# Optimization experiments

Hardware: AMD Instinct MI355X
Metric: run time of the kernel (lower is better)

Reference implementation:

```python
import jax, jax.numpy as jnp
import numpy as np

B, K_SLOTS, P = 4096, 8, 768
SLOT = P // 3          # 256, slot feature dim
HID = 256              # pres/up hidden width
NC, NP = 512, 512
LN_EPS = 1e-5


def _layernorm(x, g, b):
    m = jnp.mean(x, axis=-1, keepdims=True)
    v = jnp.var(x, axis=-1, keepdims=True)
    return (x - m) * jax.lax.rsqrt(v + LN_EPS) * g + b


def _mlp2(x, W1, b1, g, bt, W2, b2):
    # Linear -> LayerNorm -> ReLU -> Linear (torchvision ops.MLP with hidden=[256, out])
    h = jax.nn.relu(_layernorm(x @ W1 + b1, g, bt))
    return h @ W2 + b2


def setup_inputs() -> dict:
    key = jax.random.key(0)
    ks = jax.random.split(key, 24)
    rn = lambda k, shp, s=1.0: jax.random.normal(k, shp, dtype=jnp.float32) * s
    d = {
        "inst_embed": rn(ks[0], (B, P)),
        "slots": rn(ks[1], (B, K_SLOTS, SLOT)),
        # fc / fp: single Linear(p, p)
        "Wfc": rn(ks[2], (P, P), 1.0 / np.sqrt(P)),
        "bfc": jnp.zeros((P,), jnp.float32),
        "Wfp": rn(ks[3], (P, P), 1.0 / np.sqrt(P)),
        "bfp": jnp.zeros((P,), jnp.float32),
        # memory codebooks (plain randn per the original)
        "Kc": rn(ks[4], (NC, P)),
        "Vc": rn(ks[5], (NC, P)),
        "Kp": rn(ks[6], (NP, P)),
        "Vp": rn(ks[7], (NP, P)),
        # pres MLP: Linear(4p/3,256)+LN+ReLU, Linear(256,p/3)
        "pres_W1": rn(ks[8], (SLOT + P, HID), 1.0 / np.sqrt(SLOT + P)),
        "pres_b1": jnp.zeros((HID,), jnp.float32),
        "pres_g": jnp.ones((HID,), jnp.float32),
        "pres_bt": jnp.zeros((HID,), jnp.float32),
        "pres_W2": rn(ks[9], (HID, SLOT), 1.0 / np.sqrt(HID)),
        "pres_b2": jnp.zeros((SLOT,), jnp.float32),
        # up MLP: same shapes
        "up_W1": rn(ks[10], (SLOT + P, HID), 1.0 / np.sqrt(SLOT + P)),
        "up_b1": jnp.zeros((HID,), jnp.float32),
        "up_g": jnp.ones((HID,), jnp.float32),
        "up_bt": jnp.zeros((HID,), jnp.float32),
        "up_W2": rn(ks[11], (HID, SLOT), 1.0 / np.sqrt(HID)),
        "up_b2": jnp.zeros((SLOT,), jnp.float32),
    }
    return d


def reference(inst_embed, slots, Wfc, bfc, Wfp, bfp, Kc, Vc, Kp, Vp,
              pres_W1, pres_b1, pres_g, pres_bt, pres_W2, pres_b2,
              up_W1, up_b1, up_g, up_bt, up_W2, up_b2):
    scale = jnp.float32(np.sqrt(P))
    # selection: soft attention over the two codebooks
    Qc = inst_embed @ Wfc + bfc                     # [B, P]
    Qp = inst_embed @ Wfp + bfp                     # [B, P]
    c = jax.nn.softmax(jnp.einsum('bi,ci->bc', Qc, Kc) / scale, axis=-1) @ Vc  # [B, P]
    p = jax.nn.softmax(jnp.einsum('bi,pi->bp', Qp, Kp) / scale, axis=-1) @ Vp  # [B, P]
    # update: vectorized over the K slot loop of the original
    cb = jnp.broadcast_to(c[:, None, :], (B, K_SLOTS, P))
    pb = jnp.broadcast_to(p[:, None, :], (B, K_SLOTS, P))
    hc = jnp.concatenate([slots, cb], axis=-1)      # [B, K, SLOT+P]
    hp = jnp.concatenate([slots, pb], axis=-1)      # [B, K, SLOT+P]
    gate_pres = _mlp2(hc, pres_W1, pres_b1, pres_g, pres_bt, pres_W2, pres_b2)
    gate_up = _mlp2(hp, up_W1, up_b1, up_g, up_bt, up_W2, up_b2)
    return slots + gate_pres * gate_up              # [B, K, SLOT]
```

## Files before the change

kernel.cpp:

```cpp
#include <hip/hip_runtime.h>
#include <stdint.h>

#define BB    4096
#define KS    8
#define PP    768
#define SLOT  256
#define HID   256
#define NC    512
#define BKROWS (BB*KS)
typedef unsigned short u16;
typedef short bf16x8 __attribute__((ext_vector_type(8)));
typedef float f32x4  __attribute__((ext_vector_type(4)));

__device__ __forceinline__ u16 f2bf(float x) {
  union { float f; uint32_t u; } v; v.f = x;
  return (u16)((v.u + 0x7FFFu + ((v.u >> 16) & 1u)) >> 16);
}

__device__ __forceinline__ u16 f2h(float x) {
  union { _Float16 h; u16 u; } cv; cv.h = (_Float16)x; return cv.u;
}
__device__ __forceinline__ float h2f(u16 x) {
  union { u16 u; _Float16 h; } cv; cv.u = x; return (float)cv.h;
}

__device__ __forceinline__ void gload_lds16(u16* ldst, const u16* gsrc) {
  __builtin_amdgcn_global_load_lds(
      (const __attribute__((address_space(1))) void*)gsrc,
      (__attribute__((address_space(3))) void*)ldst, 16, 0, 0);
}

template<int EPI>
__device__ __forceinline__ void gemm_core6464(
    const u16* __restrict__ A, int lda,
    const u16* __restrict__ B, int ldb,
    const float* __restrict__ bias,
    void* __restrict__ out, int ldo, int K,
    int blockRow, int blockCol, u16* lsA, u16* lsB)
{
  const int tid  = threadIdx.x;
  const int w    = tid >> 6;
  const int lane = tid & 63;
  const int wm   = w >> 1, wn = w & 1;
  const int rl   = lane >> 4, cl = lane & 15;

  f32x4 acc[2][2];
  const f32x4 zero = {0.f, 0.f, 0.f, 0.f};
#pragma unroll
  for (int i = 0; i < 2; ++i)
#pragma unroll
    for (int j = 0; j < 2; ++j) acc[i][j] = zero;

  const u16* Ablk = A + (size_t)blockRow * lda;
  const u16* Bblk = B + (size_t)blockCol * ldb;

  for (int k0 = 0; k0 < K; k0 += 64) {
#pragma unroll
    for (int i = 0; i < 2; ++i) {
      int seg   = i * 4 + w;
      int off16 = seg * 64 + lane;
      int row   = off16 >> 3;
      int chunk = (off16 & 7) ^ (row & 7);
      gload_lds16(lsA + seg * 512, Ablk + (size_t)row * lda + k0 + chunk * 8);
    }
#pragma unroll
    for (int i = 0; i < 2; ++i) {
      int seg   = i * 4 + w;
      int off16 = seg * 64 + lane;
      int row   = off16 >> 3;
      int chunk = (off16 & 7) ^ (row & 7);
      gload_lds16(lsB + seg * 512, Bblk + (size_t)row * ldb + k0 + chunk * 8);
    }
    __syncthreads();

#pragma unroll
    for (int ks = 0; ks < 2; ++ks) {
      bf16x8 aF[2], bF[2];
#pragma unroll
      for (int f = 0; f < 2; ++f) {
        int r  = wm * 32 + f * 16 + cl;
        int ca = ((ks * 4 + rl) ^ (r & 7)) * 8;
        aF[f] = *(const bf16x8*)(lsA + r * 64 + ca);
        int rn = wn * 32 + f * 16 + cl;
        int cb = ((ks * 4 + rl) ^ (rn & 7)) * 8;
        bF[f] = *(const bf16x8*)(lsB + rn * 64 + cb);
      }
#pragma unroll
      for (int fm = 0; fm < 2; ++fm)
#pragma unroll
        for (int fn = 0; fn < 2; ++fn)
          acc[fm][fn] = __builtin_amdgcn_mfma_f32_16x16x32_bf16(
              aF[fm], bF[fn], acc[fm][fn], 0, 0, 0);
    }
    __syncthreads();
  }

#pragma unroll
  for (int fm = 0; fm < 2; ++fm) {
#pragma unroll
    for (int fn = 0; fn < 2; ++fn) {
      f32x4 v = acc[fm][fn];
#pragma unroll
      for (int r = 0; r < 4; ++r) {
        int grow = blockRow + wm * 32 + fm * 16 + rl * 4 + r;
        int gcol = blockCol + wn * 32 + fn * 16 + cl;
        float x = v[r];
        if constexpr (EPI == 2) {
          ((u16*)out)[(size_t)grow * ldo + gcol] = f2bf(x);
        } else if constexpr (EPI == 3) {
          x += bias[gcol];
          ((float*)out)[(size_t)grow * ldo + gcol] = x;
        } else if constexpr (EPI == 5) {
          x += bias[gcol];
          ((u16*)out)[(size_t)grow * ldo + gcol] = f2h(x);
        }
      }
    }
  }
}

__device__ __forceinline__ void cvt_seg(const float* __restrict__ in,
                                        u16* __restrict__ outp, int b, int n4) {
  int i = b * 256 + threadIdx.x;
  if (i < n4) {
    float4 v = ((const float4*)in)[i];
    ushort4 o;
    o.x = f2bf(v.x); o.y = f2bf(v.y); o.z = f2bf(v.z); o.w = f2bf(v.w);
    ((ushort4*)outp)[i] = o;
  }
}

__device__ __forceinline__ void pack_seg(const float* __restrict__ s0,
                                         const float* __restrict__ s1,
                                         u16* __restrict__ dst, int b) {
  int br = b >> 4, ng = b & 15;
  const float* src = br ? s1 : s0;
  int w = threadIdx.x >> 6, lane = threadIdx.x & 63;
  int rl = lane >> 4, cl = lane & 15;
#pragma unroll
  for (int s = 0; s < 2; ++s) {
    int step = w * 2 + s;
    union { u16 u[8]; uint4 q; } o;
#pragma unroll
    for (int j = 0; j < 8; ++j)
      o.u[j] = f2bf(src[(size_t)(step * 32 + rl * 8 + j) * 256 + ng * 16 + cl]);
    *(uint4*)(dst + (size_t)(((br * 16 + ng) * 8 + step) * 64 + lane) * 8) = o.q;
  }
}

__global__ __launch_bounds__(256) void prep_all(
    const float* __restrict__ Kc, const float* __restrict__ Kp,
    const float* __restrict__ Wfc, const float* __restrict__ Wfp,
    const float* __restrict__ Vc, const float* __restrict__ Vp,
    const float* __restrict__ pW1, const float* __restrict__ uW1,
    const float* __restrict__ pW2, const float* __restrict__ uW2,
    const float* __restrict__ bfc, const float* __restrict__ bfp,
    u16* Kcb, u16* Kpb, u16* Wfcb, u16* Wfpb, u16* Vcb, u16* Vpb,
    u16* W1Tp, u16* W1Tu, u16* W1pk, u16* W2pk, float* sb)
{
  __shared__ float tile[32][33];
  int b = blockIdx.x;
  if (b < 384)       { cvt_seg(Kc,   Kcb,   b,         98304); return; }
  else if (b < 768)  { cvt_seg(Kp,   Kpb,   b - 384,   98304); return; }
  else if (b < 1344) { cvt_seg(Wfc,  Wfcb,  b - 768,  147456); return; }
  else if (b < 1920) { cvt_seg(Wfp,  Wfpb,  b - 1344, 147456); return; }
  else if (b < 2304) { cvt_seg(Vc,   Vcb,   b - 1920,  98304); return; }
  else if (b < 2688) { cvt_seg(Vp,   Vpb,   b - 2304,  98304); return; }
  else if (b < 3200) {
    int bb = b - 2688;
    const float* in = (bb < 256) ? pW1 : uW1;
    u16* outp = (bb < 256) ? W1Tp : W1Tu;
    bb &= 255;
    int tc = (bb & 7) * 32, tr = (bb >> 3) * 32;
    int lx = threadIdx.x & 31, ly = threadIdx.x >> 5;
#pragma unroll
    for (int i = 0; i < 32; i += 8)
      tile[ly + i][lx] = in[(size_t)(tr + ly + i) * 256 + tc + lx];
    __syncthreads();
#pragma unroll
    for (int i = 0; i < 32; i += 8)
      outp[(size_t)(tc + ly + i) * 1024 + tr + lx] = f2bf(tile[lx][ly + i]);
    return;
  }
  else if (b < 3232) { pack_seg(pW1, uW1, W1pk, b - 3200); return; }
  else if (b < 3264) { pack_seg(pW2, uW2, W2pk, b - 3232); return; }
  else {
    int w = threadIdx.x >> 6, lane = threadIdx.x & 63;
    int row = (b - 3264) * 4 + w;
    int br = row >> 9, n = row & 511;
    const float* Kr = (br ? Kp : Kc) + (size_t)n * PP;
    const float* bf = br ? bfp : bfc;
    float s = 0.f;
#pragma unroll
    for (int j = 0; j < 12; ++j) s += Kr[lane + j * 64] * bf[lane + j * 64];
#pragma unroll
    for (int o = 32; o; o >>= 1) s += __shfl_xor(s, o);
    if (!lane) sb[row] = s;
  }
}

__global__ __launch_bounds__(256) void gemm_mixed(
    const u16* Kcb, const u16* Kpb, const u16* Wfcb, const u16* Wfpb,
    u16* KWc, u16* KWp,
    const u16* W1Tp, const u16* W1Tu, const u16* Vcb, const u16* Vpb,
    u16* VW1p, u16* VW1u)
{
  __shared__ u16 lsA[64 * 64];
  __shared__ u16 lsB[64 * 64];
  int b = blockIdx.x;
  if (b < 192) {
    int z = b / 96, r = b % 96;
    gemm_core6464<2>(z ? Kpb : Kcb, PP, z ? Wfpb : Wfcb, PP, nullptr,
                     z ? KWp : KWc, PP, PP, (r & 7) * 64, (r >> 3) * 64, lsA, lsB);
  } else {
    int c = b - 192, z = c / 32, r = c % 32;
    gemm_core6464<2>((z ? W1Tu : W1Tp) + 256, 1024, z ? Vpb : Vcb, PP, nullptr,
                     z ? VW1u : VW1p, NC, PP, (r & 3) * 64, (r >> 2) * 64, lsA, lsB);
  }
}

__global__ __launch_bounds__(256) void gemm_scores(
    const float* __restrict__ inst, const u16* __restrict__ KW,
    const float* __restrict__ sb, u16* __restrict__ scH)
{
  __shared__ u16 lsA[64 * 64];
  __shared__ u16 lsB[64 * 64];
  const int tid  = threadIdx.x;
  const int w    = tid >> 6;
  const int lane = tid & 63;
  const int wm   = w >> 1, wn = w & 1;
  const int rl   = lane >> 4, cl = lane & 15;
  const int blockRow = blockIdx.x * 64;
  const int blockCol = blockIdx.y * 64;

  const int arow = tid >> 2;
  const int kseg = (tid & 3) * 16;

  f32x4 acc[2][2];
  const f32x4 zero = {0.f, 0.f, 0.f, 0.f};
#pragma unroll
  for (int i = 0; i < 2; ++i)
#pragma unroll
    for (int j = 0; j < 2; ++j) acc[i][j] = zero;

  const float* Asrc = inst + (size_t)(blockRow + arow) * PP + kseg;
  const u16*   Bblk = KW + (size_t)blockCol * PP;

  for (int k0 = 0; k0 < PP; k0 += 64) {
    union { u16 u[8]; uint4 q; } c0, c1;
#pragma unroll
    for (int j = 0; j < 2; ++j) {
      float4 v0 = *(const float4*)(Asrc + k0 + j * 8);
      float4 v1 = *(const float4*)(Asrc + k0 + j * 8 + 4);
      u16* dd = j ? c1.u : c0.u;
      dd[0] = f2bf(v0.x); dd[1] = f2bf(v0.y); dd[2] = f2bf(v0.z); dd[3] = f2bf(v0.w);
      dd[4] = f2bf(v1.x); dd[5] = f2bf(v1.y); dd[6] = f2bf(v1.z); dd[7] = f2bf(v1.w);
    }
    int cc = kseg >> 3;
    *(uint4*)(lsA + arow * 64 + (((cc     ) ^ (arow & 7)) << 3)) = c0.q;
    *(uint4*)(lsA + arow * 64 + (((cc + 1) ^ (arow & 7)) << 3)) = c1.q;
#pragma unroll
    for (int i = 0; i < 2; ++i) {
      int seg   = i * 4 + w;
      int off16 = seg * 64 + lane;
      int row   = off16 >> 3;
      int chunk = (off16 & 7) ^ (row & 7);
      gload_lds16(lsB + seg * 512, Bblk + (size_t)row * PP + k0 + chunk * 8);
    }
    __syncthreads();

#pragma unroll
    for (int ks = 0; ks < 2; ++ks) {
      bf16x8 aF[2], bF[2];
#pragma unroll
      for (int f = 0; f < 2; ++f) {
        int r  = wm * 32 + f * 16 + cl;
        int ca = ((ks * 4 + rl) ^ (r & 7)) * 8;
        aF[f] = *(const bf16x8*)(lsA + r * 64 + ca);
        int rn = wn * 32 + f * 16 + cl;
        int cb = ((ks * 4 + rl) ^ (rn & 7)) * 8;
        bF[f] = *(const bf16x8*)(lsB + rn * 64 + cb);
      }
#pragma unroll
      for (int fm = 0; fm < 2; ++fm)
#pragma unroll
        for (int fn = 0; fn < 2; ++fn)
          acc[fm][fn] = __builtin_amdgcn_mfma_f32_16x16x32_bf16(
              aF[fm], bF[fn], acc[fm][fn], 0, 0, 0);
    }
    __syncthreads();
  }

#pragma unroll
  for (int fm = 0; fm < 2; ++fm)
#pragma unroll
    for (int fn = 0; fn < 2; ++fn) {
      f32x4 v = acc[fm][fn];
#pragma unroll
      for (int r = 0; r < 4; ++r) {
        int grow = blockRow + wm * 32 + fm * 16 + rl * 4 + r;
        int gcol = blockCol + wn * 32 + fn * 16 + cl;
        scH[(size_t)grow * 1024 + gcol] = f2h(v[r] + sb[gcol]);
      }
    }
}

__global__ __launch_bounds__(256) void gemm_t(
    const u16* Pb, const u16* VW1p, const u16* VW1u,
    const float* pb1, const float* ub1, float* t0, float* t1)
{
  __shared__ u16 lsA[64 * 64];
  __shared__ u16 lsB[64 * 64];
  int z = blockIdx.z;
  gemm_core6464<3>(Pb + (size_t)z * BB * NC, NC, z ? VW1u : VW1p, NC,
                   z ? ub1 : pb1, z ? t1 : t0, SLOT, NC,
                   blockIdx.x * 64, blockIdx.y * 64, lsA, lsB);
}

__global__ __launch_bounds__(256) void softmax_rows(const u16* __restrict__ scH,
                                                    u16* __restrict__ Pp) {
  int w = threadIdx.x >> 6, lane = threadIdx.x & 63;
  int row = blockIdx.x * 4 + w;
  int i = row >> 1, b = row & 1;
  const u16* src = scH + (size_t)i * 1024 + b * 512 + lane * 8;
  uint4 q = *(const uint4*)src;
  const u16* hp = (const u16*)&q;
  float vv[8];
#pragma unroll
  for (int j = 0; j < 8; ++j) vv[j] = h2f(hp[j]);
  float m = vv[0];
#pragma unroll
  for (int j = 1; j < 8; ++j) m = fmaxf(m, vv[j]);
#pragma unroll
  for (int o = 32; o; o >>= 1) m = fmaxf(m, __shfl_xor(m, o));
  const float alpha = 0.03608439182435161f;
  float e[8], s = 0.f;
#pragma unroll
  for (int j = 0; j < 8; ++j) { e[j] = __expf((vv[j] - m) * alpha); s += e[j]; }
#pragma unroll
  for (int o = 32; o; o >>= 1) s += __shfl_xor(s, o);
  float inv = 1.f / s;
  union { u16 u[8]; uint4 q; } ou;
#pragma unroll
  for (int j = 0; j < 8; ++j) ou.u[j] = f2bf(e[j] * inv);
  *(uint4*)(Pp + ((size_t)b * BB + i) * 512 + lane * 8) = ou.q;
}

__global__ __launch_bounds__(512, 4) void fused_update(
    const float* __restrict__ slots,
    const float* __restrict__ t0, const float* __restrict__ t1,
    const u16* __restrict__ W1pk, const u16* __restrict__ W2pk,
    const float* __restrict__ pg, const float* __restrict__ pbt,
    const float* __restrict__ ug, const float* __restrict__ ubt,
    const float* __restrict__ pb2, const float* __restrict__ ub2,
    float* __restrict__ outp)
{
  __shared__ u16 lsH[2][32 * 256];
  __shared__ float lstat[2][32][16];
  __shared__ float lfin[2][32][2];

  const int tid = threadIdx.x, w = tid >> 6, lane = tid & 63;
  const int rl = lane >> 4, cl = lane & 15;
  const int blockRow = blockIdx.x * 32;

  u16* lsA = lsH[0];

#pragma unroll
  for (int it = 0; it < 4; ++it) {
    int L = it * 512 + tid;
    int row = L >> 6, qc = L & 63;
    float4 v = *(const float4*)(slots + (size_t)(blockRow + row) * 256 + qc * 4);
    ushort4 b; b.x = f2bf(v.x); b.y = f2bf(v.y); b.z = f2bf(v.z); b.w = f2bf(v.w);
    int chunk = qc >> 1, half = qc & 1;
    *(ushort4*)(lsA + row * 256 + (((chunk ^ (row & 7)) << 3) + half * 4)) = b;
  }

  float tp_[2][2], tu_[2][2];
#pragma unroll
  for (int fm = 0; fm < 2; ++fm) {
    size_t trr = (size_t)(blockIdx.x * 4 + fm * 2 + (rl >> 1)) * 256;
#pragma unroll
    for (int fn = 0; fn < 2; ++fn) {
      int col = w * 32 + fn * 16 + cl;
      tp_[fm][fn] = t0[trr + col];
      tu_[fm][fn] = t1[trr + col];
    }
  }

#define MF(A, B, C) C = __builtin_amdgcn_mfma_f32_16x16x32_bf16(A, B, C, 0, 0, 0);

  bf16x8 pb[3][2], ub[3][2];
#define FR1(NG, S) (*(const bf16x8*)(W1pk + (size_t)(((NG) * 8 + (S)) * 64 + lane) * 8))
#define LDW1(SL, S) { pb[SL][0] = FR1(w * 2, S);      pb[SL][1] = FR1(w * 2 + 1, S);  \
                      ub[SL][0] = FR1(16 + w * 2, S); ub[SL][1] = FR1(17 + w * 2, S); \
                      asm volatile("" ::: "memory"); }
  LDW1(0, 0) LDW1(1, 1) LDW1(2, 2)
  __syncthreads();

  f32x4 acc[2][4];
  const f32x4 zero = {0.f, 0.f, 0.f, 0.f};
#pragma unroll
  for (int i = 0; i < 2; ++i)
#pragma unroll
    for (int j = 0; j < 4; ++j) acc[i][j] = zero;

#pragma unroll
  for (int s = 0; s < 8; ++s) {
    const int sl = s % 3;
    bf16x8 a0 = *(const bf16x8*)(lsA + cl * 256 + (((s * 4 + rl) ^ (cl & 7)) << 3));
    bf16x8 a1 = *(const bf16x8*)(lsA + (16 + cl) * 256 + (((s * 4 + rl) ^ (cl & 7)) << 3));
    MF(a0, pb[sl][0], acc[0][0]) MF(a1, pb[sl][0], acc[1][0])
    MF(a0, pb[sl][1], acc[0][1]) MF(a1, pb[sl][1], acc[1][1])
    MF(a0, ub[sl][0], acc[0][2]) MF(a1, ub[sl][0], acc[1][2])
    MF(a0, ub[sl][1], acc[0][3]) MF(a1, ub[sl][1], acc[1][3])
    if (s < 5) LDW1(sl, s + 3)
  }
#undef LDW1
#undef FR1

#pragma unroll
  for (int fm = 0; fm < 2; ++fm)
#pragma unroll
    for (int fn = 0; fn < 2; ++fn)
#pragma unroll
      for (int r = 0; r < 4; ++r) {
        acc[fm][fn][r]     += tp_[fm][fn];
        acc[fm][2 + fn][r] += tu_[fm][fn];
      }

#pragma unroll
  for (int fm = 0; fm < 2; ++fm)
#pragma unroll
    for (int br = 0; br < 2; ++br) {
      f32x4 s = acc[fm][br * 2] + acc[fm][br * 2 + 1];
      f32x4 q = acc[fm][br * 2] * acc[fm][br * 2] + acc[fm][br * 2 + 1] * acc[fm][br * 2 + 1];
#pragma unroll
      for (int o = 1; o < 16; o <<= 1) {
#pragma unroll
        for (int r = 0; r < 4; ++r) {
          s[r] += __shfl_xor(s[r], o);
          q[r] += __shfl_xor(q[r], o);
        }
      }
      if (cl == 0) {
#pragma unroll
        for (int r = 0; r < 4; ++r) {
          int row = fm * 16 + rl * 4 + r;
          lstat[br][row][w]     = s[r];
          lstat[br][row][8 + w] = q[r];
        }
      }
    }
  __syncthreads();

  if (tid < 64) {
    int fb = tid >> 5, row = tid & 31;
    f32x4 a = *(const f32x4*)&lstat[fb][row][0];
    f32x4 b = *(const f32x4*)&lstat[fb][row][4];
    f32x4 c = *(const f32x4*)&lstat[fb][row][8];
    f32x4 d = *(const f32x4*)&lstat[fb][row][12];
    float ss = a[0] + a[1] + a[2] + a[3] + b[0] + b[1] + b[2] + b[3];
    float qq = c[0] + c[1] + c[2] + c[3] + d[0] + d[1] + d[2] + d[3];
    float mu = ss * (1.f / 256.f);
    lfin[fb][row][0] = mu;
    lfin[fb][row][1] = rsqrtf(qq * (1.f / 256.f) - mu * mu + 1e-5f);
  }
  __syncthreads();

  const int brw = w >> 2, wc = w & 3;
  const u16* hsrc = lsH[brw];
  const float* b2src = brw ? ub2 : pb2;
  float b2v[4];
#pragma unroll
  for (int fn = 0; fn < 4; ++fn) b2v[fn] = b2src[wc * 64 + fn * 16 + cl];

  bf16x8 bq[3][4];
#define FR2(NG, S) (*(const bf16x8*)(W2pk + (size_t)(((NG) * 8 + (S)) * 64 + lane) * 8))
#define LDW2(SL, S) { bq[SL][0] = FR2(brw * 16 + wc * 4,     S); \
                      bq[SL][1] = FR2(brw * 16 + wc * 4 + 1, S); \
                      bq[SL][2] = FR2(brw * 16 + wc * 4 + 2, S); \
                      bq[SL][3] = FR2(brw * 16 + wc * 4 + 3, S); \
                      asm volatile("" ::: "memory"); }
  LDW2(0, 0)

  {
    float gv[2][2], btv[2][2];
#pragma unroll
    for (int fn = 0; fn < 2; ++fn) {
      int col = w * 32 + fn * 16 + cl;
      gv[0][fn] = pg[col];  btv[0][fn] = pbt[col];
      gv[1][fn] = ug[col];  btv[1][fn] = ubt[col];
    }
#pragma unroll
    for (int fm = 0; fm < 2; ++fm) {
      float mean[2][4], rstd[2][4];
#pragma unroll
      for (int r = 0; r < 4; ++r) {
        int row = fm * 16 + rl * 4 + r;
        mean[0][r] = lfin[0][row][0]; rstd[0][r] = lfin[0][row][1];
        mean[1][r] = lfin[1][row][0]; rstd[1][r] = lfin[1][row][1];
      }
#pragma unroll
      for (int br = 0; br < 2; ++br)
#pragma unroll
        for (int fn = 0; fn < 2; ++fn) {
          int col = w * 32 + fn * 16 + cl;
#pragma unroll
          for (int r = 0; r < 4; ++r) {
            int row = fm * 16 + rl * 4 + r;
            float h = fmaxf((acc[fm][br * 2 + fn][r] - mean[br][r]) * rstd[br][r]
                            * gv[br][fn] + btv[br][fn], 0.f);
            lsH[br][row * 256 + (((col >> 3) ^ (row & 7)) << 3) + (col & 7)] = f2bf(h);
          }
        }
    }
  }
#pragma unroll
  for (int i = 0; i < 2; ++i)
#pragma unroll
    for (int j = 0; j < 4; ++j) acc[i][j] = zero;
  __syncthreads();

  LDW2(1, 1) LDW2(2, 2)
#pragma unroll
  for (int s = 0; s < 8; ++s) {
    const int sl = s % 3;
    bf16x8 a0 = *(const bf16x8*)(hsrc + cl * 256 + (((s * 4 + rl) ^ (cl & 7)) << 3));
    bf16x8 a1 = *(const bf16x8*)(hsrc + (16 + cl) * 256 + (((s * 4 + rl) ^ (cl & 7)) << 3));
    MF(a0, bq[sl][0], acc[0][0]) MF(a1, bq[sl][0], acc[1][0])
    MF(a0, bq[sl][1], acc[0][1]) MF(a1, bq[sl][1], acc[1][1])
    MF(a0, bq[sl][2], acc[0][2]) MF(a1, bq[sl][2], acc[1][2])
    MF(a0, bq[sl][3], acc[0][3]) MF(a1, bq[sl][3], acc[1][3])
    if (s < 5) LDW2(sl, s + 3)
  }
#undef LDW2
#undef FR2
#undef MF
  __syncthreads();

  float* xbuf = (float*)&lsH[0][0];
  const int base = wc * 2048;
  if (brw == 0) {
#pragma unroll
    for (int fm = 0; fm < 2; ++fm)
#pragma unroll
      for (int fn = 0; fn < 4; ++fn)
#pragma unroll
        for (int r = 0; r < 4; ++r)
          xbuf[base + ((fm * 4 + fn) * 4 + r) * 64 + lane] = acc[fm][fn][r] + b2v[fn];
  }
  __syncthreads();

  if (brw == 1) {
#pragma unroll
    for (int fm = 0; fm < 2; ++fm)
#pragma unroll
      for (int fn = 0; fn < 4; ++fn)
#pragma unroll
        for (int r = 0; r < 4; ++r) {
          float gp = xbuf[base + ((fm * 4 + fn) * 4 + r) * 64 + lane];
          float gu = acc[fm][fn][r] + b2v[fn];
          int row = blockRow + fm * 16 + rl * 4 + r;
          int col = wc * 64 + fn * 16 + cl;
          size_t idx = (size_t)row * 256 + col;
          outp[idx] = slots[idx] + gp * gu;
        }
  }
}

extern "C" void kernel_launch(void* const* d_in, const int* in_sizes, int n_in,
                              void* d_out, int out_size, void* d_ws, size_t ws_size,
                              hipStream_t stream) {
  const float* inst  = (const float*)d_in[0];
  const float* slots = (const float*)d_in[1];
  const float* Wfc   = (const float*)d_in[2];
  const float* bfc   = (const float*)d_in[3];
  const float* Wfp   = (const float*)d_in[4];
  const float* bfp   = (const float*)d_in[5];
  const float* Kc    = (const float*)d_in[6];
  const float* Vc    = (const float*)d_in[7];
  const float* Kp    = (const float*)d_in[8];
  const float* Vp    = (const float*)d_in[9];
  const float* pW1   = (const float*)d_in[10];
  const float* pb1   = (const float*)d_in[11];
  const float* pg    = (const float*)d_in[12];
  const float* pbt   = (const float*)d_in[13];
  const float* pW2   = (const float*)d_in[14];
  const float* pb2   = (const float*)d_in[15];
  const float* uW1   = (const float*)d_in[16];
  const float* ub1   = (const float*)d_in[17];
  const float* ug    = (const float*)d_in[18];
  const float* ubt   = (const float*)d_in[19];
  const float* uW2   = (const float*)d_in[20];
  const float* ub2   = (const float*)d_in[21];
  float* out = (float*)d_out;
  char*  ws  = (char*)d_ws;

  const size_t OFF_KC    = 0;
  const size_t OFF_KP    = OFF_KC    + 786432;
  const size_t OFF_WFCB  = OFF_KP    + 786432;
  const size_t OFF_WFPB  = OFF_WFCB  + 1179648;
  const size_t OFF_VCB   = OFF_WFPB  + 1179648;
  const size_t OFF_VPB   = OFF_VCB   + 786432;
  const size_t OFF_W1TP  = OFF_VPB   + 786432;
  const size_t OFF_W1TU  = OFF_W1TP  + 524288;
  const size_t OFF_W1PK  = OFF_W1TU  + 524288;
  const size_t OFF_W2PK  = OFF_W1PK  + 262144;
  const size_t OFF_KW    = OFF_W2PK  + 262144;
  const size_t OFF_VW1   = OFF_KW    + 1572864;
  const size_t OFF_SB    = OFF_VW1   + 524288;
  const size_t OFF_T     = OFF_SB    + 4096;
  const size_t OFF_SC    = OFF_T     + 8388608;
  const size_t OFF_P     = OFF_SC    + 8388608;

  u16*   Kcb   = (u16*)(ws + OFF_KC);
  u16*   Kpb   = (u16*)(ws + OFF_KP);
  u16*   Wfcb  = (u16*)(ws + OFF_WFCB);
  u16*   Wfpb  = (u16*)(ws + OFF_WFPB);
  u16*   Vcb   = (u16*)(ws + OFF_VCB);
  u16*   Vpb   = (u16*)(ws + OFF_VPB);
  u16*   W1Tp  = (u16*)(ws + OFF_W1TP);
  u16*   W1Tu  = (u16*)(ws + OFF_W1TU);
  u16*   W1pk  = (u16*)(ws + OFF_W1PK);
  u16*   W2pk  = (u16*)(ws + OFF_W2PK);
  u16*   KWc   = (u16*)(ws + OFF_KW);
  u16*   KWp   = KWc + (size_t)NC * PP;
  u16*   VW1p  = (u16*)(ws + OFF_VW1);
  u16*   VW1u  = VW1p + (size_t)SLOT * NC;
  float* sb    = (float*)(ws + OFF_SB);
  float* t0    = (float*)(ws + OFF_T);
  float* t1    = t0 + (size_t)BB * SLOT;
  u16*   scH   = (u16*)(ws + OFF_SC);
  u16*   Pb    = (u16*)(ws + OFF_P);

  prep_all<<<dim3(3520), 256, 0, stream>>>(
      Kc, Kp, Wfc, Wfp, Vc, Vp, pW1, uW1, pW2, uW2, bfc, bfp,
      Kcb, Kpb, Wfcb, Wfpb, Vcb, Vpb, W1Tp, W1Tu, W1pk, W2pk, sb);

  gemm_mixed<<<dim3(256), 256, 0, stream>>>(
      Kcb, Kpb, Wfcb, Wfpb, KWc, KWp, W1Tp, W1Tu, Vcb, Vpb, VW1p, VW1u);

  gemm_scores<<<dim3(64, 16), 256, 0, stream>>>(inst, KWc, sb, scH);

  softmax_rows<<<dim3(2048), 256, 0, stream>>>(scH, Pb);

  gemm_t<<<dim3(64, 4, 2), 256, 0, stream>>>(Pb, VW1p, VW1u, pb1, ub1, t0, t1);

  fused_update<<<dim3(1024), 512, 0, stream>>>(
      slots, t0, t1, W1pk, W2pk, pg, pbt, ug, ubt, pb2, ub2, out);

  (void)in_sizes; (void)n_in; (void)out_size; (void)ws_size;
}
```

Measured before the change: 90.50 us.

## Fuse softmax into P·VW1 GEMM and pre-convert inst to bf16

Drops the standalone softmax kernel. The second GEMM now reads fp16 scores, computes the row softmax into a 64x512 bf16 LDS tile, and runs the MFMA loop against VW1 from that tile, so the probability matrix no longer makes a round trip through global memory. The score GEMM now takes inst already converted to bf16 in the prep kernel and reuses the generic gemm_core with an epilogue variant. In exchange, the softmax is recomputed by each of the 4 column blocks per row, the fused kernel uses much more LDS (about 72KB), and prep gains a larger conversion pass.

```diff
diff --git a/kernel.cpp b/kernel.cpp
--- a/kernel.cpp
+++ b/kernel.cpp
@@ -149,25 +149,27 @@
 }
 
 __global__ __launch_bounds__(256) void prep_all(
-    const float* __restrict__ Kc, const float* __restrict__ Kp,
-    const float* __restrict__ Wfc, const float* __restrict__ Wfp,
-    const float* __restrict__ Vc, const float* __restrict__ Vp,
-    const float* __restrict__ pW1, const float* __restrict__ uW1,
-    const float* __restrict__ pW2, const float* __restrict__ uW2,
-    const float* __restrict__ bfc, const float* __restrict__ bfp,
-    u16* Kcb, u16* Kpb, u16* Wfcb, u16* Wfpb, u16* Vcb, u16* Vpb,
+    const float* __restrict__ inst, const float* __restrict__ Kc,
+    const float* __restrict__ Kp, const float* __restrict__ Wfc,
+    const float* __restrict__ Wfp, const float* __restrict__ Vc,
+    const float* __restrict__ Vp, const float* __restrict__ pW1,
+    const float* __restrict__ uW1, const float* __restrict__ pW2,
+    const float* __restrict__ uW2, const float* __restrict__ bfc,
+    const float* __restrict__ bfp,
+    u16* instb, u16* Kcb, u16* Kpb, u16* Wfcb, u16* Wfpb, u16* Vcb, u16* Vpb,
     u16* W1Tp, u16* W1Tu, u16* W1pk, u16* W2pk, float* sb)
 {
   __shared__ float tile[32][33];
   int b = blockIdx.x;
-  if (b < 384)       { cvt_seg(Kc,   Kcb,   b,         98304); return; }
-  else if (b < 768)  { cvt_seg(Kp,   Kpb,   b - 384,   98304); return; }
-  else if (b < 1344) { cvt_seg(Wfc,  Wfcb,  b - 768,  147456); return; }
-  else if (b < 1920) { cvt_seg(Wfp,  Wfpb,  b - 1344, 147456); return; }
-  else if (b < 2304) { cvt_seg(Vc,   Vcb,   b - 1920,  98304); return; }
-  else if (b < 2688) { cvt_seg(Vp,   Vpb,   b - 2304,  98304); return; }
-  else if (b < 3200) {
-    int bb = b - 2688;
+  if (b < 3072)      { cvt_seg(inst, instb, b,        786432); return; }
+  else if (b < 3456) { cvt_seg(Kc,   Kcb,   b - 3072,  98304); return; }
+  else if (b < 3840) { cvt_seg(Kp,   Kpb,   b - 3456,  98304); return; }
+  else if (b < 4416) { cvt_seg(Wfc,  Wfcb,  b - 3840, 147456); return; }
+  else if (b < 4992) { cvt_seg(Wfp,  Wfpb,  b - 4416, 147456); return; }
+  else if (b < 5376) { cvt_seg(Vc,   Vcb,   b - 4992,  98304); return; }
+  else if (b < 5760) { cvt_seg(Vp,   Vpb,   b - 5376,  98304); return; }
+  else if (b < 6272) {
+    int bb = b - 5760;
     const float* in = (bb < 256) ? pW1 : uW1;
     u16* outp = (bb < 256) ? W1Tp : W1Tu;
     bb &= 255;
@@ -182,11 +184,11 @@
       outp[(size_t)(tc + ly + i) * 1024 + tr + lx] = f2bf(tile[lx][ly + i]);
     return;
   }
-  else if (b < 3232) { pack_seg(pW1, uW1, W1pk, b - 3200); return; }
-  else if (b < 3264) { pack_seg(pW2, uW2, W2pk, b - 3232); return; }
+  else if (b < 6304) { pack_seg(pW1, uW1, W1pk, b - 6272); return; }
+  else if (b < 6336) { pack_seg(pW2, uW2, W2pk, b - 6304); return; }
   else {
     int w = threadIdx.x >> 6, lane = threadIdx.x & 63;
-    int row = (b - 3264) * 4 + w;
+    int row = (b - 6336) * 4 + w;
     int br = row >> 9, n = row & 511;
     const float* Kr = (br ? Kp : Kc) + (size_t)n * PP;
     const float* bf = br ? bfp : bfc;
@@ -220,21 +222,56 @@
 }
 
 __global__ __launch_bounds__(256) void gemm_scores(
-    const float* __restrict__ inst, const u16* __restrict__ KW,
-    const float* __restrict__ sb, u16* __restrict__ scH)
+    const u16* instb, const u16* KW, const float* sb, u16* scH)
 {
   __shared__ u16 lsA[64 * 64];
   __shared__ u16 lsB[64 * 64];
-  const int tid  = threadIdx.x;
-  const int w    = tid >> 6;
-  const int lane = tid & 63;
-  const int wm   = w >> 1, wn = w & 1;
-  const int rl   = lane >> 4, cl = lane & 15;
+  gemm_core6464<5>(instb, PP, KW, PP, sb, scH, 1024, PP,
+                   blockIdx.x * 64, blockIdx.y * 64, lsA, lsB);
+}
+
+__global__ __launch_bounds__(256) void gemm_t_fused(
+    const u16* __restrict__ scH,
+    const u16* __restrict__ VW1p, const u16* __restrict__ VW1u,
+    const float* __restrict__ pb1, const float* __restrict__ ub1,
+    float* __restrict__ t0, float* __restrict__ t1)
+{
+  __shared__ u16 lsP[64 * 512];
+  __shared__ u16 lsB[64 * 64];
+  const int z = blockIdx.z;
+  const int tid = threadIdx.x, w = tid >> 6, lane = tid & 63;
+  const int wm = w >> 1, wn = w & 1;
+  const int rl = lane >> 4, cl = lane & 15;
   const int blockRow = blockIdx.x * 64;
   const int blockCol = blockIdx.y * 64;
 
-  const int arow = tid >> 2;
-  const int kseg = (tid & 3) * 16;
+  const float alpha = 0.03608439182435161f;
+#pragma unroll
+  for (int it = 0; it < 16; ++it) {
+    int row = it * 4 + w;
+    const u16* src = scH + (size_t)(blockRow + row) * 1024 + z * 512 + lane * 8;
+    uint4 q = *(const uint4*)src;
+    const u16* hp = (const u16*)&q;
+    float vv[8];
+#pragma unroll
+    for (int j = 0; j < 8; ++j) vv[j] = h2f(hp[j]);
+    float m = vv[0];
+#pragma unroll
+    for (int j = 1; j < 8; ++j) m = fmaxf(m, vv[j]);
+#pragma unroll
+    for (int o = 32; o; o >>= 1) m = fmaxf(m, __shfl_xor(m, o));
+    float e[8], s = 0.f;
+#pragma unroll
+    for (int j = 0; j < 8; ++j) { e[j] = __expf((vv[j] - m) * alpha); s += e[j]; }
+#pragma unroll
+    for (int o = 32; o; o >>= 1) s += __shfl_xor(s, o);
+    float inv = 1.f / s;
+    union { u16 u[8]; uint4 q; } ou;
+#pragma unroll
+    for (int j = 0; j < 8; ++j) ou.u[j] = f2bf(e[j] * inv);
+    *(uint4*)(lsP + row * 512 + ((lane ^ (row & 7)) << 3)) = ou.q;
+  }
+  __syncthreads();
 
   f32x4 acc[2][2];
   const f32x4 zero = {0.f, 0.f, 0.f, 0.f};
@@ -243,40 +280,25 @@
 #pragma unroll
     for (int j = 0; j < 2; ++j) acc[i][j] = zero;
 
-  const float* Asrc = inst + (size_t)(blockRow + arow) * PP + kseg;
-  const u16*   Bblk = KW + (size_t)blockCol * PP;
-
-  for (int k0 = 0; k0 < PP; k0 += 64) {
-    union { u16 u[8]; uint4 q; } c0, c1;
-#pragma unroll
-    for (int j = 0; j < 2; ++j) {
-      float4 v0 = *(const float4*)(Asrc + k0 + j * 8);
-      float4 v1 = *(const float4*)(Asrc + k0 + j * 8 + 4);
-      u16* dd = j ? c1.u : c0.u;
-      dd[0] = f2bf(v0.x); dd[1] = f2bf(v0.y); dd[2] = f2bf(v0.z); dd[3] = f2bf(v0.w);
-      dd[4] = f2bf(v1.x); dd[5] = f2bf(v1.y); dd[6] = f2bf(v1.z); dd[7] = f2bf(v1.w);
-    }
-    int cc = kseg >> 3;
-    *(uint4*)(lsA + arow * 64 + (((cc     ) ^ (arow & 7)) << 3)) = c0.q;
-    *(uint4*)(lsA + arow * 64 + (((cc + 1) ^ (arow & 7)) << 3)) = c1.q;
+  const u16* Bblk = (z ? VW1u : VW1p) + (size_t)blockCol * NC;
+  for (int k0 = 0; k0 < NC; k0 += 64) {
 #pragma unroll
     for (int i = 0; i < 2; ++i) {
       int seg   = i * 4 + w;
       int off16 = seg * 64 + lane;
       int row   = off16 >> 3;
       int chunk = (off16 & 7) ^ (row & 7);
-      gload_lds16(lsB + seg * 512, Bblk + (size_t)row * PP + k0 + chunk * 8);
+      gload_lds16(lsB + seg * 512, Bblk + (size_t)row * NC + k0 + chunk * 8);
     }
     __syncthreads();
-
 #pragma unroll
     for (int ks = 0; ks < 2; ++ks) {
       bf16x8 aF[2], bF[2];
 #pragma unroll
       for (int f = 0; f < 2; ++f) {
         int r  = wm * 32 + f * 16 + cl;
-        int ca = ((ks * 4 + rl) ^ (r & 7)) * 8;
-        aF[f] = *(const bf16x8*)(lsA + r * 64 + ca);
+        int cc = (k0 >> 3) + ks * 4 + rl;
+        aF[f] = *(const bf16x8*)(lsP + r * 512 + ((cc ^ (r & 7)) << 3));
         int rn = wn * 32 + f * 16 + cl;
         int cb = ((ks * 4 + rl) ^ (rn & 7)) * 8;
         bF[f] = *(const bf16x8*)(lsB + rn * 64 + cb);
@@ -291,6 +313,8 @@
     __syncthreads();
   }
 
+  const float* bias = z ? ub1 : pb1;
+  float* outp = z ? t1 : t0;
 #pragma unroll
   for (int fm = 0; fm < 2; ++fm)
 #pragma unroll
@@ -300,50 +324,9 @@
       for (int r = 0; r < 4; ++r) {
         int grow = blockRow + wm * 32 + fm * 16 + rl * 4 + r;
         int gcol = blockCol + wn * 32 + fn * 16 + cl;
-        scH[(size_t)grow * 1024 + gcol] = f2h(v[r] + sb[gcol]);
-      }
-    }
-}
-
-__global__ __launch_bounds__(256) void gemm_t(
-    const u16* Pb, const u16* VW1p, const u16* VW1u,
-    const float* pb1, const float* ub1, float* t0, float* t1)
-{
-  __shared__ u16 lsA[64 * 64];
-  __shared__ u16 lsB[64 * 64];
-  int z = blockIdx.z;
-  gemm_core6464<3>(Pb + (size_t)z * BB * NC, NC, z ? VW1u : VW1p, NC,
-                   z ? ub1 : pb1, z ? t1 : t0, SLOT, NC,
-                   blockIdx.x * 64, blockIdx.y * 64, lsA, lsB);
-}
-
-__global__ __launch_bounds__(256) void softmax_rows(const u16* __restrict__ scH,
-                                                    u16* __restrict__ Pp) {
-  int w = threadIdx.x >> 6, lane = threadIdx.x & 63;
-  int row = blockIdx.x * 4 + w;
-  int i = row >> 1, b = row & 1;
-  const u16* src = scH + (size_t)i * 1024 + b * 512 + lane * 8;
-  uint4 q = *(const uint4*)src;
-  const u16* hp = (const u16*)&q;
-  float vv[8];
-#pragma unroll
-  for (int j = 0; j < 8; ++j) vv[j] = h2f(hp[j]);
-  float m = vv[0];
-#pragma unroll
-  for (int j = 1; j < 8; ++j) m = fmaxf(m, vv[j]);
-#pragma unroll
-  for (int o = 32; o; o >>= 1) m = fmaxf(m, __shfl_xor(m, o));
-  const float alpha = 0.03608439182435161f;
-  float e[8], s = 0.f;
-#pragma unroll
-  for (int j = 0; j < 8; ++j) { e[j] = __expf((vv[j] - m) * alpha); s += e[j]; }
-#pragma unroll
-  for (int o = 32; o; o >>= 1) s += __shfl_xor(s, o);
-  float inv = 1.f / s;
-  union { u16 u[8]; uint4 q; } ou;
-#pragma unroll
-  for (int j = 0; j < 8; ++j) ou.u[j] = f2bf(e[j] * inv);
-  *(uint4*)(Pp + ((size_t)b * BB + i) * 512 + lane * 8) = ou.q;
+        outp[(size_t)grow * SLOT + gcol] = v[r] + bias[gcol];
+      }
+    }
 }
 
 __global__ __launch_bounds__(512, 4) void fused_update(
@@ -596,7 +579,8 @@
   float* out = (float*)d_out;
   char*  ws  = (char*)d_ws;
 
-  const size_t OFF_KC    = 0;
+  const size_t OFF_INST  = 0;
+  const size_t OFF_KC    = OFF_INST  + 6291456;
   const size_t OFF_KP    = OFF_KC    + 786432;
   const size_t OFF_WFCB  = OFF_KP    + 786432;
   const size_t OFF_WFPB  = OFF_WFCB  + 1179648;
@@ -611,8 +595,8 @@
   const size_t OFF_SB    = OFF_VW1   + 524288;
   const size_t OFF_T     = OFF_SB    + 4096;
   const size_t OFF_SC    = OFF_T     + 8388608;
-  const size_t OFF_P     = OFF_SC    + 8388608;
-
+
+  u16*   instb = (u16*)(ws + OFF_INST);
   u16*   Kcb   = (u16*)(ws + OFF_KC);
   u16*   Kpb   = (u16*)(ws + OFF_KP);
   u16*   Wfcb  = (u16*)(ws + OFF_WFCB);
@@ -631,20 +615,18 @@
   float* t0    = (float*)(ws + OFF_T);
   float* t1    = t0 + (size_t)BB * SLOT;
   u16*   scH   = (u16*)(ws + OFF_SC);
-  u16*   Pb    = (u16*)(ws + OFF_P);
-
-  prep_all<<<dim3(3520), 256, 0, stream>>>(
-      Kc, Kp, Wfc, Wfp, Vc, Vp, pW1, uW1, pW2, uW2, bfc, bfp,
-      Kcb, Kpb, Wfcb, Wfpb, Vcb, Vpb, W1Tp, W1Tu, W1pk, W2pk, sb);
+
+  prep_all<<<dim3(6592), 256, 0, stream>>>(
+      inst, Kc, Kp, Wfc, Wfp, Vc, Vp, pW1, uW1, pW2, uW2, bfc, bfp,
+      instb, Kcb, Kpb, Wfcb, Wfpb, Vcb, Vpb, W1Tp, W1Tu, W1pk, W2pk, sb);
 
   gemm_mixed<<<dim3(256), 256, 0, stream>>>(
       Kcb, Kpb, Wfcb, Wfpb, KWc, KWp, W1Tp, W1Tu, Vcb, Vpb, VW1p, VW1u);
 
-  gemm_scores<<<dim3(64, 16), 256, 0, stream>>>(inst, KWc, sb, scH);
-
-  softmax_rows<<<dim3(2048), 256, 0, stream>>>(scH, Pb);
-
-  gemm_t<<<dim3(64, 4, 2), 256, 0, stream>>>(Pb, VW1p, VW1u, pb1, ub1, t0, t1);
+  gemm_scores<<<dim3(64, 16), 256, 0, stream>>>(instb, KWc, sb, scH);
+
+  gemm_t_fused<<<dim3(64, 4, 2), 256, 0, stream>>>(
+      scH, VW1p, VW1u, pb1, ub1, t0, t1);
 
   fused_update<<<dim3(1024), 512, 0, stream>>>(
       slots, t0, t1, W1pk, W2pk, pg, pbt, ug, ubt, pb2, ub2, out);
```

After: 89.13 us. No clear change (-1.5%).
